# Kernel tuning notes

Measured on AMD Instinct MI355X. Metric: run time of the kernel, lower is better.

Reference implementation:

```python
import jax, jax.numpy as jnp
import numpy as np

N, E, DIN, DL, DOUT, G, K = 50000, 800000, 32, 128, 10, 256, 3


def setup_inputs() -> dict:
    key = jax.random.key(0)
    ks = jax.random.split(key, 24)
    rn = lambda k, s: jax.random.normal(k, s, jnp.float32) * 0.05
    inp = {}
    inp["x"] = jax.random.normal(ks[0], (N, DIN), jnp.float32)
    inp["edge_index"] = jax.random.randint(ks[1], (2, E), 0, N, jnp.int32)
    inp["batch_ids"] = jnp.sort(jax.random.randint(ks[2], (N,), 0, G, jnp.int32))
    inp["y"] = jax.random.uniform(ks[3], (G, DOUT), dtype=jnp.float32)
    inp["eps"] = jax.random.uniform(ks[4], (K, N, DL), dtype=jnp.float32)  # torch.rand_like -> uniform
    inp["W_in"] = rn(ks[5], (DIN, DL)); inp["b_in"] = jnp.zeros((DL,), jnp.float32)
    inp["W_gcn"] = rn(ks[6], (DL, DL)); inp["b_gcn"] = jnp.zeros((DL,), jnp.float32)
    inp["W_enc"] = rn(ks[7], (5, DL, DL)); inp["b_enc"] = jnp.zeros((5, DL), jnp.float32)
    inp["W_mu"] = rn(ks[8], (DL, DL)); inp["b_mu"] = jnp.zeros((DL,), jnp.float32)
    inp["W_std"] = rn(ks[9], (DL, DL)); inp["b_std"] = jnp.zeros((DL,), jnp.float32)
    dims = [DL, 256, 128, 64, 32, 16]
    for i in range(5):
        inp[f"Wd{i}"] = rn(ks[10 + i], (dims[i], dims[i + 1]))
        inp[f"bd{i}"] = jnp.zeros((dims[i + 1],), jnp.float32)
    inp["Wo"] = rn(ks[15], (16, DOUT)); inp["bo"] = jnp.zeros((DOUT,), jnp.float32)
    inp["k"] = K
    return inp


def reference(x, edge_index, batch_ids, y, eps, W_in, b_in, W_gcn, b_gcn,
              W_enc, b_enc, W_mu, b_mu, W_std, b_std,
              Wd0, bd0, Wd1, bd1, Wd2, bd2, Wd3, bd3, Wd4, bd4, Wo, bo, k):
    n = x.shape[0]
    src, dst = edge_index[0], edge_index[1]
    # GCN symmetric normalization with self-loops (PyG gcn_norm, edge_weight=1)
    deg = jnp.zeros((n,), x.dtype).at[dst].add(1.0) + 1.0  # +1 for self-loop
    dinv = jax.lax.rsqrt(deg)
    enorm = (dinv[src] * dinv[dst])[:, None]  # [E,1]
    snorm = (dinv * dinv)[:, None]            # [N,1] self-loop norm

    h = jax.nn.sigmoid(x @ W_in + b_in)  # input layer
    mu = h; std = h
    for i in range(k):  # k hops of MPEncoder (shared weights)
        g = h @ W_gcn  # [N,DL]
        g = jax.ops.segment_sum(g[src] * enorm, dst, num_segments=n) + g * snorm + b_gcn
        for j in range(5):
            g = jax.nn.sigmoid(g @ W_enc[j] + b_enc[j])
        mu = g @ W_mu + b_mu
        std = jax.nn.softplus(g @ W_std + b_std - 5.0)
        h = mu + std * eps[i]  # reparametrization with uniform noise

    # Decoder MLP per node, sigmoid output
    d = h
    for Wd, bd in ((Wd0, bd0), (Wd1, bd1), (Wd2, bd2), (Wd3, bd3), (Wd4, bd4)):
        d = jax.nn.relu(d @ Wd + bd)
    yp = jax.nn.sigmoid(d @ Wo + bo)  # [N,DOUT]

    # global_mean_pool over graphs
    g_count = y.shape[0]
    sums = jax.ops.segment_sum(yp, batch_ids, num_segments=g_count)
    cnt = jax.ops.segment_sum(jnp.ones((n,), yp.dtype), batch_ids, num_segments=g_count)
    y_pred = sums / jnp.maximum(cnt, 1.0)[:, None]
    return (y_pred, mu, std, y)
```

## Files before the change

### kernel.cpp

```cpp
#include <hip/hip_runtime.h>
#include <math.h>

#define DIN 32
#define DL 128
#define DOUT 10

typedef _Float16 f16x8 __attribute__((ext_vector_type(8)));
typedef float f32x4 __attribute__((ext_vector_type(4)));

__device__ __forceinline__ float sigm(float x){ return 1.0f/(1.0f+expf(-x)); }
__device__ __forceinline__ float softplus_(float x){ return fmaxf(x,0.0f) + log1pf(expf(-fabsf(x))); }

__global__ void count_edges_k(const int* __restrict__ ei, int* __restrict__ cnt, int E){
    int e = blockIdx.x*256 + threadIdx.x;
    if (e < E) atomicAdd(&cnt[ei[E + e]], 1);
}

__global__ void dinv_k(const int* __restrict__ cnt, float* __restrict__ dinv, int N){
    int i = blockIdx.x*256 + threadIdx.x;
    if (i < N) dinv[i] = rsqrtf((float)cnt[i] + 1.0f);
}

__global__ void block_sum_k(const int* __restrict__ cnt, int* __restrict__ bsum, int n){
    __shared__ int ws_[4];
    int tid = threadIdx.x;
    int i = blockIdx.x*256 + tid;
    int v = (i < n) ? cnt[i] : 0;
    #pragma unroll
    for (int off = 32; off > 0; off >>= 1) v += __shfl_xor(v, off);
    if ((tid & 63) == 0) ws_[tid >> 6] = v;
    __syncthreads();
    if (tid == 0) bsum[blockIdx.x] = ws_[0] + ws_[1] + ws_[2] + ws_[3];
}

__global__ void scan_bsum_k(int* __restrict__ bsum, int nb){
    __shared__ int tmp[1024];
    int tid = threadIdx.x;
    int v = (tid < nb) ? bsum[tid] : 0;
    tmp[tid] = v; __syncthreads();
    for (int off = 1; off < 1024; off <<= 1){
        int t = (tid >= off) ? tmp[tid-off] : 0;
        __syncthreads();
        tmp[tid] += t;
        __syncthreads();
    }
    if (tid < nb) bsum[tid] = tmp[tid] - v;
}

__global__ void block_scan_k(const int* __restrict__ cnt, const int* __restrict__ bexcl,
                             int* __restrict__ cursor, int* __restrict__ rowptr, int n){
    __shared__ int tmp[256];
    int tid = threadIdx.x;
    int i = blockIdx.x*256 + tid;
    int v = (i < n) ? cnt[i] : 0;
    tmp[tid] = v; __syncthreads();
    for (int off = 1; off < 256; off <<= 1){
        int t = (tid >= off) ? tmp[tid-off] : 0;
        __syncthreads();
        tmp[tid] += t;
        __syncthreads();
    }
    int excl = bexcl[blockIdx.x] + tmp[tid] - v;
    if (i < n){ cursor[i] = excl; rowptr[i+1] = excl + v; }
    if (i == 0) rowptr[0] = 0;
}

__global__ void place_edges_k(const int* __restrict__ ei, int* __restrict__ cursor,
                              int* __restrict__ csr_src, int E){
    int e = blockIdx.x*256 + threadIdx.x;
    if (e < E){
        int s = ei[e], d = ei[E + e];
        csr_src[atomicAdd(&cursor[d], 1)] = s;
    }
}

struct WPA { const float* s; _Float16* d; int K; int C; };
struct WPA14 { WPA a[14]; };
__global__ void wprep_all_k(WPA14 args){
    WPA w = args.a[blockIdx.y];
    int idx = blockIdx.x*256 + threadIdx.x;
    if (idx < w.K*w.C){ int k = idx / w.C, c = idx % w.C; w.d[(size_t)c*w.K + k] = (_Float16)w.s[idx]; }
}

template<int K, int NC16, bool ZERO>
__device__ __forceinline__ void mfma_ldsmm(const _Float16* As, int lda,
        const _Float16* Ws, int ldw, f32x4 (&acc)[2][8], int ln, int q, int wid){
    if (ZERO){
        #pragma unroll
        for (int r = 0; r < 2; ++r)
            #pragma unroll
            for (int c = 0; c < 8; ++c) acc[r][c] = (f32x4){0.f,0.f,0.f,0.f};
    }
    #pragma unroll
    for (int kk = 0; kk < K/32; ++kk){
        int ko = kk*32 + q*8;
        f16x8 a0 = *(const f16x8*)&As[(size_t)(wid*32 + ln)*lda + ko];
        f16x8 a1 = *(const f16x8*)&As[(size_t)(wid*32 + 16 + ln)*lda + ko];
        #pragma unroll
        for (int c = 0; c < NC16; ++c){
            f16x8 b = *(const f16x8*)&Ws[(size_t)(c*16 + ln)*ldw + ko];
            acc[0][c] = __builtin_amdgcn_mfma_f32_16x16x32_f16(a0, b, acc[0][c], 0, 0, 0);
            acc[1][c] = __builtin_amdgcn_mfma_f32_16x16x32_f16(a1, b, acc[1][c], 0, 0, 0);
        }
    }
}

template<int NC16, int ACT>
__device__ __forceinline__ void act_store_lds(_Float16* D, int ldd, f32x4 (&acc)[2][8],
        const float* bias, int ln, int q, int wid){
    #pragma unroll
    for (int r = 0; r < 2; ++r){
        int rowb = wid*32 + r*16 + q*4;
        #pragma unroll
        for (int c = 0; c < NC16; ++c){
            int col = c*16 + ln;
            float bv = bias ? bias[col] : 0.0f;
            #pragma unroll
            for (int i2 = 0; i2 < 4; ++i2){
                float v = acc[r][c][i2] + bv;
                if (ACT == 1) v = sigm(v);
                else if (ACT == 2) v = fmaxf(v, 0.0f);
                D[(size_t)(rowb + i2)*ldd + col] = (_Float16)v;
            }
        }
    }
}

__device__ __forceinline__ void stage_w(const _Float16* Wg, _Float16* Wl, int ldw,
                                        int C, int K, int tid){
    int kq = K/8, tot = C*kq;
    for (int i = tid; i < tot; i += 256){
        int r = i/kq, s = i%kq;
        *(f16x8*)&Wl[(size_t)r*ldw + s*8] = *(const f16x8*)&Wg[(size_t)r*K + s*8];
    }
}

__device__ __forceinline__ void pf_load_w(const _Float16* Wg, f16x8 (&pf)[8], int tid){
    #pragma unroll
    for (int i = 0; i < 8; ++i) pf[i] = *(const f16x8*)&Wg[(size_t)(tid + i*256)*8];
}
__device__ __forceinline__ void pf_store_w(_Float16* Wl, f16x8 (&pf)[8], int tid){
    #pragma unroll
    for (int i = 0; i < 8; ++i){
        int g = tid + i*256; int r = g >> 4, s = g & 15;
        *(f16x8*)&Wl[(size_t)r*136 + s*8] = pf[i];
    }
}

__global__ __launch_bounds__(256,1) void fused_input_k(const float* __restrict__ x,
        const _Float16* __restrict__ WtIN, const float* __restrict__ b_in,
        const _Float16* __restrict__ WtGCN, _Float16* __restrict__ gOut, int nrows){
    __shared__ __align__(16) _Float16 Ax[128*40];
    __shared__ __align__(16) _Float16 Hl[128*136];
    __shared__ __align__(16) _Float16 Wi[128*40];
    __shared__ __align__(16) _Float16 Wg[128*136];
    int tid = threadIdx.x, lane = tid & 63, wid = tid >> 6;
    int ln = lane & 15, q = lane >> 4;
    int row0 = blockIdx.x * 128;
    for (int i = tid; i < 512; i += 256){
        int r = i >> 2, s = i & 3;
        f16x8 v = {};
        if (row0 + r < nrows){
            const float* xs = &x[(size_t)(row0+r)*DIN + s*8];
            float4 u0 = *(const float4*)xs, u1 = *(const float4*)(xs+4);
            v[0]=(_Float16)u0.x; v[1]=(_Float16)u0.y; v[2]=(_Float16)u0.z; v[3]=(_Float16)u0.w;
            v[4]=(_Float16)u1.x; v[5]=(_Float16)u1.y; v[6]=(_Float16)u1.z; v[7]=(_Float16)u1.w;
        }
        *(f16x8*)&Ax[r*40 + s*8] = v;
        *(f16x8*)&Wi[r*40 + s*8] = *(const f16x8*)&WtIN[(size_t)r*32 + s*8];
    }
    for (int i = tid; i < 2048; i += 256){
        int r = i >> 4, s = i & 15;
        *(f16x8*)&Wg[r*136 + s*8] = *(const f16x8*)&WtGCN[(size_t)r*128 + s*8];
    }
    __syncthreads();
    f32x4 acc[2][8];
    mfma_ldsmm<32,8,true>(Ax, 40, Wi, 40, acc, ln, q, wid);
    act_store_lds<8,1>(Hl, 136, acc, b_in, ln, q, wid);
    __syncthreads();
    mfma_ldsmm<128,8,true>(Hl, 136, Wg, 136, acc, ln, q, wid);
    #pragma unroll
    for (int r = 0; r < 2; ++r){
        int rowb = row0 + wid*32 + r*16 + q*4;
        #pragma unroll
        for (int c = 0; c < 8; ++c){
            int col = c*16 + ln;
            #pragma unroll
            for (int i2 = 0; i2 < 4; ++i2){
                int row = rowb + i2;
                if (row < nrows) gOut[(size_t)row*DL + col] = (_Float16)acc[r][c][i2];
            }
        }
    }
}

__global__ __launch_bounds__(256) void gcn_agg_h(const _Float16* __restrict__ g,
        _Float16* __restrict__ out, const int* __restrict__ rowptr,
        const int* __restrict__ csr_src, const float* __restrict__ dinv,
        const float* __restrict__ bgcn, int N){
    int t = threadIdx.x;
    int node = blockIdx.x*16 + (t >> 4);
    int f = (t & 15)*8;
    if (node >= N) return;
    float dv = dinv[node];
    float sn = dv*dv;
    f16x8 sv = *(const f16x8*)&g[(size_t)node*DL + f];
    float acc[8];
    #pragma unroll
    for (int j = 0; j < 8; ++j) acc[j] = (float)sv[j]*sn + bgcn[f+j];
    int e0 = rowptr[node], e1 = rowptr[node+1];
    for (int e = e0; e < e1; ++e){
        int s = csr_src[e];
        float w = dinv[s]*dv;
        f16x8 nv = *(const f16x8*)&g[(size_t)s*DL + f];
        #pragma unroll
        for (int j = 0; j < 8; ++j) acc[j] += (float)nv[j]*w;
    }
    f16x8 o;
    #pragma unroll
    for (int j = 0; j < 8; ++j) o[j] = (_Float16)acc[j];
    *(f16x8*)&out[(size_t)node*DL + f] = o;
}

template<int LAST>
__global__ __launch_bounds__(256,1) void fused_hop_k(const _Float16* __restrict__ g2,
        const _Float16* __restrict__ Wt8, const float* __restrict__ b_enc,
        const float* __restrict__ b_mu, const float* __restrict__ b_std,
        const float* __restrict__ eps_i, _Float16* __restrict__ gOut,
        float* __restrict__ muOut, float* __restrict__ stdOut,
        _Float16* __restrict__ hOut, int nrows){
    __shared__ __align__(16) _Float16 actA[128*136];
    __shared__ __align__(16) _Float16 actB[128*136];
    __shared__ __align__(16) _Float16 wb[2][128*136];
    int tid = threadIdx.x, lane = tid & 63, wid = tid >> 6;
    int ln = lane & 15, q = lane >> 4;
    int row0 = blockIdx.x * 128;
    for (int i = tid; i < 2048; i += 256){
        int r = i >> 4, s = i & 15;
        f16x8 v = {};
        if (row0 + r < nrows) v = *(const f16x8*)&g2[(size_t)(row0+r)*DL + s*8];
        *(f16x8*)&actA[r*136 + s*8] = v;
        *(f16x8*)&wb[0][r*136 + s*8] = *(const f16x8*)&Wt8[(size_t)1*16384 + (size_t)r*128 + s*8];
    }
    __syncthreads();
    _Float16* src = actA; _Float16* dst = actB;
    int cur = 0;
    f32x4 acc[2][8], accS[2][8];
    f16x8 pf[8];
    #pragma unroll 1
    for (int j = 0; j < 5; ++j){
        const _Float16* nxtW = Wt8 + (size_t)((j < 4) ? (2+j) : 6)*16384;
        pf_load_w(nxtW, pf, tid);
        mfma_ldsmm<128,8,true>(src, 136, wb[cur], 136, acc, ln, q, wid);
        pf_store_w(wb[cur^1], pf, tid);
        act_store_lds<8,1>(dst, 136, acc, b_enc + j*DL, ln, q, wid);
        cur ^= 1;
        { _Float16* t = src; src = dst; dst = t; }
        __syncthreads();
    }
    pf_load_w(Wt8 + (size_t)7*16384, pf, tid);
    mfma_ldsmm<128,8,true>(src, 136, wb[cur], 136, acc, ln, q, wid);
    pf_store_w(wb[cur^1], pf, tid);
    cur ^= 1;
    __syncthreads();
    if (!LAST) pf_load_w(Wt8, pf, tid);
    mfma_ldsmm<128,8,true>(src, 136, wb[cur], 136, accS, ln, q, wid);
    if (!LAST) pf_store_w(wb[cur^1], pf, tid);
    cur ^= 1;
    #pragma unroll
    for (int r = 0; r < 2; ++r){
        int rowb = wid*32 + r*16 + q*4;
        #pragma unroll
        for (int c = 0; c < 8; ++c){
            int col = c*16 + ln;
            float bm = b_mu[col], bs = b_std[col];
            #pragma unroll
            for (int i2 = 0; i2 < 4; ++i2){
                int row = rowb + i2;
                int grow = row0 + row;
                float mv = acc[r][c][i2] + bm;
                float sv = softplus_(accS[r][c][i2] + bs - 5.0f);
                float ev = (grow < nrows) ? eps_i[(size_t)grow*DL + col] : 0.0f;
                float hv = mv + sv*ev;
                if (LAST){
                    if (grow < nrows){
                        muOut[(size_t)grow*DL + col] = mv;
                        stdOut[(size_t)grow*DL + col] = sv;
                        hOut[(size_t)grow*DL + col] = (_Float16)hv;
                    }
                } else {
                    dst[(size_t)row*136 + col] = (_Float16)hv;
                }
            }
        }
    }
    if (!LAST){
        __syncthreads();
        mfma_ldsmm<128,8,true>(dst, 136, wb[cur], 136, acc, ln, q, wid);
        #pragma unroll
        for (int r = 0; r < 2; ++r){
            int rowb = row0 + wid*32 + r*16 + q*4;
            #pragma unroll
            for (int c = 0; c < 8; ++c){
                int col = c*16 + ln;
                #pragma unroll
                for (int i2 = 0; i2 < 4; ++i2){
                    int row = rowb + i2;
                    if (row < nrows) gOut[(size_t)row*DL + col] = (_Float16)acc[r][c][i2];
                }
            }
        }
    }
}

__global__ __launch_bounds__(256,1) void decoder_k(const _Float16* __restrict__ h,
        const _Float16* __restrict__ WtD0, const _Float16* __restrict__ WtD1,
        const _Float16* __restrict__ WtD2, const _Float16* __restrict__ WtD3,
        const _Float16* __restrict__ WtD4,
        const float* __restrict__ bd0, const float* __restrict__ bd1,
        const float* __restrict__ bd2, const float* __restrict__ bd3,
        const float* __restrict__ bd4, const float* __restrict__ Wo,
        const float* __restrict__ bo, const int* __restrict__ batch,
        float* __restrict__ sums, float* __restrict__ gcnt, int nrows){
    __shared__ __align__(16) _Float16 A[128*136];
    __shared__ __align__(16) _Float16 B[128*264];
    __shared__ __align__(16) _Float16 W[128*136];
    __shared__ float WoL[16*DOUT];
    __shared__ float boL[DOUT];
    int tid = threadIdx.x, lane = tid & 63, wid = tid >> 6;
    int ln = lane & 15, q = lane >> 4;
    int row0 = blockIdx.x * 128;
    for (int i = tid; i < 2048; i += 256){
        int r = i >> 4, s = i & 15;
        f16x8 v = {};
        if (row0 + r < nrows) v = *(const f16x8*)&h[(size_t)(row0+r)*DL + s*8];
        *(f16x8*)&A[r*136 + s*8] = v;
    }
    if (tid < 16*DOUT) WoL[tid] = Wo[tid];
    if (tid < DOUT) boL[tid] = bo[tid];
    f32x4 acc[2][8];
    for (int ch = 0; ch < 2; ++ch){
        stage_w(WtD0 + (size_t)ch*128*128, W, 136, 128, 128, tid);
        __syncthreads();
        mfma_ldsmm<128,8,true>(A, 136, W, 136, acc, ln, q, wid);
        act_store_lds<8,2>(B + ch*128, 264, acc, bd0 + ch*128, ln, q, wid);
        __syncthreads();
    }
    for (int kh = 0; kh < 2; ++kh){
        for (int i = tid; i < 2048; i += 256){
            int r = i >> 4, s = i & 15;
            *(f16x8*)&W[r*136 + s*8] = *(const f16x8*)&WtD1[(size_t)r*256 + kh*128 + s*8];
        }
        __syncthreads();
        if (kh == 0) mfma_ldsmm<128,8,true >(B,       264, W, 136, acc, ln, q, wid);
        else         mfma_ldsmm<128,8,false>(B + 128, 264, W, 136, acc, ln, q, wid);
        __syncthreads();
    }
    act_store_lds<8,2>(A, 136, acc, bd1, ln, q, wid);
    __syncthreads();
    stage_w(WtD2, W, 136, 64, 128, tid);
    __syncthreads();
    mfma_ldsmm<128,4,true>(A, 136, W, 136, acc, ln, q, wid);
    act_store_lds<4,2>(B, 264, acc, bd2, ln, q, wid);
    __syncthreads();
    stage_w(WtD3, W, 136, 32, 64, tid);
    __syncthreads();
    mfma_ldsmm<64,2,true>(B, 264, W, 136, acc, ln, q, wid);
    act_store_lds<2,2>(A, 136, acc, bd3, ln, q, wid);
    __syncthreads();
    stage_w(WtD4, W, 136, 16, 32, tid);
    __syncthreads();
    mfma_ldsmm<32,1,true>(A, 136, W, 136, acc, ln, q, wid);
    act_store_lds<1,2>(B, 264, acc, bd4, ln, q, wid);
    __syncthreads();
    int node = row0 + tid;
    bool valid = (tid < 128) && (node < nrows);
    float yp[DOUT];
    int b = -1;
    if (valid){
        float dd[16];
        #pragma unroll
        for (int k = 0; k < 16; ++k) dd[k] = (float)B[(size_t)tid*264 + k];
        #pragma unroll
        for (int o = 0; o < DOUT; ++o){
            float a2 = boL[o];
            #pragma unroll
            for (int k = 0; k < 16; ++k) a2 += dd[k]*WoL[k*DOUT + o];
            yp[o] = sigm(a2);
        }
        b = batch[node];
    }
    int b0 = __builtin_amdgcn_readfirstlane(b);
    unsigned long long m = __ballot(b == b0);
    if (m == ~0ull && b0 >= 0){
        #pragma unroll
        for (int o = 0; o < DOUT; ++o){
            float v = yp[o];
            for (int off = 32; off > 0; off >>= 1) v += __shfl_xor(v, off);
            if ((tid & 63) == 0) atomicAdd(&sums[b0*DOUT + o], v);
        }
        if ((tid & 63) == 0) atomicAdd(&gcnt[b0], 64.0f);
    } else if (valid){
        #pragma unroll
        for (int o = 0; o < DOUT; ++o) atomicAdd(&sums[b*DOUT + o], yp[o]);
        atomicAdd(&gcnt[b], 1.0f);
    }
}

__global__ void divide_k(float* __restrict__ out, const float* __restrict__ gcnt, int n){
    int i = blockIdx.x*256 + threadIdx.x;
    if (i < n) out[i] = out[i] / fmaxf(gcnt[i/DOUT], 1.0f);
}

__global__ void copy_k(const float* __restrict__ src, float* __restrict__ dst, int n){
    int i = blockIdx.x*256 + threadIdx.x;
    if (i < n) dst[i] = src[i];
}

extern "C" void kernel_launch(void* const* d_in, const int* in_sizes, int n_in,
                              void* d_out, int out_size, void* d_ws, size_t ws_size,
                              hipStream_t stream) {
    const float* x     = (const float*)d_in[0];
    const int*   ei    = (const int*)d_in[1];
    const int*   batch = (const int*)d_in[2];
    const float* y     = (const float*)d_in[3];
    const float* eps   = (const float*)d_in[4];
    const float* W_in  = (const float*)d_in[5];
    const float* b_in  = (const float*)d_in[6];
    const float* W_gcn = (const float*)d_in[7];
    const float* b_gcn = (const float*)d_in[8];
    const float* W_enc = (const float*)d_in[9];
    const float* b_enc = (const float*)d_in[10];
    const float* W_mu  = (const float*)d_in[11];
    const float* b_mu  = (const float*)d_in[12];
    const float* W_std = (const float*)d_in[13];
    const float* b_std = (const float*)d_in[14];
    const float* Wd0 = (const float*)d_in[15]; const float* bd0 = (const float*)d_in[16];
    const float* Wd1 = (const float*)d_in[17]; const float* bd1 = (const float*)d_in[18];
    const float* Wd2 = (const float*)d_in[19]; const float* bd2 = (const float*)d_in[20];
    const float* Wd3 = (const float*)d_in[21]; const float* bd3 = (const float*)d_in[22];
    const float* Wd4 = (const float*)d_in[23]; const float* bd4 = (const float*)d_in[24];
    const float* Wo  = (const float*)d_in[25]; const float* bo  = (const float*)d_in[26];

    const int N = in_sizes[2];
    const int E = in_sizes[1]/2;
    const int G = in_sizes[3]/DOUT;
    const int KHOP = in_sizes[4] / (N*DL);
    const size_t NN = (size_t)N*DL;

    char* p = (char*)d_ws;
    auto take = [&p](size_t bytes) -> char* {
        char* r = p; p += (bytes + 255) & ~(size_t)255; return r;
    };
    _Float16* hG  = (_Float16*)take(NN*2);
    _Float16* hG2 = (_Float16*)take(NN*2);
    _Float16* hH  = (_Float16*)take(NN*2);
    float* dinv  = (float*)take((size_t)N*4);
    float* gcnt  = (float*)take((size_t)G*4);
    int* cnt     = (int*)take((size_t)N*4);
    int* rowptr  = (int*)take((size_t)(N+1)*4);
    int* cursor  = (int*)take((size_t)N*4);
    int* csr_src = (int*)take((size_t)E*4);
    int* bsum    = (int*)take(1024*4);
    _Float16* Wt8  = (_Float16*)take((size_t)8*DL*DL*2);
    _Float16* WtIN = (_Float16*)take((size_t)DL*DIN*2);
    _Float16* WtD0 = (_Float16*)take((size_t)256*128*2);
    _Float16* WtD1 = (_Float16*)take((size_t)128*256*2);
    _Float16* WtD2 = (_Float16*)take((size_t)64*128*2);
    _Float16* WtD3 = (_Float16*)take((size_t)32*64*2);
    _Float16* WtD4 = (_Float16*)take((size_t)16*32*2);

    float* out_ypred = (float*)d_out;
    float* out_mu    = out_ypred + (size_t)G*DOUT;
    float* out_std   = out_mu + NN;
    float* out_y     = out_std + NN;

    hipMemsetAsync(cnt, 0, sizeof(int)*N, stream);
    hipMemsetAsync(out_ypred, 0, sizeof(float)*G*DOUT, stream);
    hipMemsetAsync(gcnt, 0, sizeof(float)*G, stream);

    int gE = (E + 255)/256, gN = (N + 255)/256;
    int nb = gN;

    count_edges_k<<<gE, 256, 0, stream>>>(ei, cnt, E);
    dinv_k<<<gN, 256, 0, stream>>>(cnt, dinv, N);
    block_sum_k<<<nb, 256, 0, stream>>>(cnt, bsum, N);
    scan_bsum_k<<<1, 1024, 0, stream>>>(bsum, nb);
    block_scan_k<<<nb, 256, 0, stream>>>(cnt, bsum, cursor, rowptr, N);
    place_edges_k<<<gE, 256, 0, stream>>>(ei, cursor, csr_src, E);

    WPA14 wa;
    wa.a[0]  = { W_in,  WtIN, DIN, DL };
    wa.a[1]  = { W_gcn, Wt8,  DL, DL };
    for (int j = 0; j < 5; ++j) wa.a[2+j] = { W_enc + (size_t)j*DL*DL, Wt8 + (size_t)(1+j)*DL*DL, DL, DL };
    wa.a[7]  = { W_mu,  Wt8 + (size_t)6*DL*DL, DL, DL };
    wa.a[8]  = { W_std, Wt8 + (size_t)7*DL*DL, DL, DL };
    wa.a[9]  = { Wd0, WtD0, 128, 256 };
    wa.a[10] = { Wd1, WtD1, 256, 128 };
    wa.a[11] = { Wd2, WtD2, 128, 64 };
    wa.a[12] = { Wd3, WtD3, 64, 32 };
    wa.a[13] = { Wd4, WtD4, 32, 16 };
    wprep_all_k<<<dim3(128, 14), 256, 0, stream>>>(wa);

    int ntile = (N + 127)/128;
    fused_input_k<<<ntile, 256, 0, stream>>>(x, WtIN, b_in, Wt8, hG, N);

    for (int i = 0; i < KHOP; ++i){
        gcn_agg_h<<<(N+15)/16, 256, 0, stream>>>(hG, hG2, rowptr, csr_src, dinv, b_gcn, N);
        const float* eps_i = eps + (size_t)i*NN;
        if (i == KHOP-1)
            fused_hop_k<1><<<ntile, 256, 0, stream>>>(hG2, Wt8, b_enc, b_mu, b_std, eps_i,
                                                      nullptr, out_mu, out_std, hH, N);
        else
            fused_hop_k<0><<<ntile, 256, 0, stream>>>(hG2, Wt8, b_enc, b_mu, b_std, eps_i,
                                                      hG, nullptr, nullptr, nullptr, N);
    }

    decoder_k<<<ntile, 256, 0, stream>>>(hH, WtD0, WtD1, WtD2, WtD3, WtD4,
                                         bd0, bd1, bd2, bd3, bd4, Wo, bo,
                                         batch, out_ypred, gcnt, N);
    divide_k<<<(G*DOUT+255)/256, 256, 0, stream>>>(out_ypred, gcnt, G*DOUT);
    copy_k<<<(G*DOUT+255)/256, 256, 0, stream>>>(y, out_y, G*DOUT);
}
```

Before: 969.8 us.

## Read weights from global memory in MFMA GEMMs and shrink LDS for higher occupancy

The MFMA matmul helper now streams weight fragments straight from global memory (L2-cached) instead of staging them in LDS. This removes the weight LDS buffers and lets the fused input and hop kernels use 512 threads with 4 blocks per CU, each wave computing a 64x32 output tile. The decoder is retiled to 64-row blocks with smaller LDS footprints, and the GCN aggregation unrolls neighbour gathers by four to expose more memory-level parallelism. The cost is repeated global or L2 traffic for weights on every block, and outputs are now staged through LDS before a coalesced copy-out.

```diff
diff --git a/kernel.cpp b/kernel.cpp
--- a/kernel.cpp
+++ b/kernel.cpp
@@ -82,83 +82,91 @@
     if (idx < w.K*w.C){ int k = idx / w.C, c = idx % w.C; w.d[(size_t)c*w.K + k] = (_Float16)w.s[idx]; }
 }
 
-template<int K, int NC16, bool ZERO>
-__device__ __forceinline__ void mfma_ldsmm(const _Float16* As, int lda,
-        const _Float16* Ws, int ldw, f32x4 (&acc)[2][8], int ln, int q, int wid){
+template<int KCH, bool ZERO>
+__device__ __forceinline__ void mm_gw(const _Float16* As, const _Float16* __restrict__ Wt,
+        int ldw, int koff, f32x4 (&acc)[4][2], int ln, int q, int rg, int cg, int ncols){
     if (ZERO){
         #pragma unroll
-        for (int r = 0; r < 2; ++r)
+        for (int mf = 0; mf < 4; ++mf)
             #pragma unroll
-            for (int c = 0; c < 8; ++c) acc[r][c] = (f32x4){0.f,0.f,0.f,0.f};
-    }
-    #pragma unroll
-    for (int kk = 0; kk < K/32; ++kk){
-        int ko = kk*32 + q*8;
-        f16x8 a0 = *(const f16x8*)&As[(size_t)(wid*32 + ln)*lda + ko];
-        f16x8 a1 = *(const f16x8*)&As[(size_t)(wid*32 + 16 + ln)*lda + ko];
-        #pragma unroll
-        for (int c = 0; c < NC16; ++c){
-            f16x8 b = *(const f16x8*)&Ws[(size_t)(c*16 + ln)*ldw + ko];
-            acc[0][c] = __builtin_amdgcn_mfma_f32_16x16x32_f16(a0, b, acc[0][c], 0, 0, 0);
-            acc[1][c] = __builtin_amdgcn_mfma_f32_16x16x32_f16(a1, b, acc[1][c], 0, 0, 0);
-        }
-    }
-}
-
-template<int NC16, int ACT>
-__device__ __forceinline__ void act_store_lds(_Float16* D, int ldd, f32x4 (&acc)[2][8],
-        const float* bias, int ln, int q, int wid){
-    #pragma unroll
-    for (int r = 0; r < 2; ++r){
-        int rowb = wid*32 + r*16 + q*4;
-        #pragma unroll
-        for (int c = 0; c < NC16; ++c){
-            int col = c*16 + ln;
-            float bv = bias ? bias[col] : 0.0f;
+            for (int cf = 0; cf < 2; ++cf) acc[mf][cf] = (f32x4){0.f,0.f,0.f,0.f};
+    }
+    #pragma unroll
+    for (int kk = 0; kk < KCH; ++kk){
+        f16x8 a[4], b[2];
+        #pragma unroll
+        for (int mf = 0; mf < 4; ++mf)
+            a[mf] = *(const f16x8*)&As[(rg*64 + mf*16 + ln)*136 + kk*32 + q*8];
+        #pragma unroll
+        for (int cf = 0; cf < 2; ++cf){
+            int col = cg*32 + cf*16 + ln;
+            if (cg*32 + cf*16 < ncols)
+                b[cf] = *(const f16x8*)&Wt[(size_t)col*ldw + koff + kk*32 + q*8];
+        }
+        #pragma unroll
+        for (int mf = 0; mf < 4; ++mf)
             #pragma unroll
-            for (int i2 = 0; i2 < 4; ++i2){
-                float v = acc[r][c][i2] + bv;
-                if (ACT == 1) v = sigm(v);
-                else if (ACT == 2) v = fmaxf(v, 0.0f);
-                D[(size_t)(rowb + i2)*ldd + col] = (_Float16)v;
+            for (int cf = 0; cf < 2; ++cf)
+                if (cg*32 + cf*16 < ncols)
+                    acc[mf][cf] = __builtin_amdgcn_mfma_f32_16x16x32_f16(a[mf], b[cf], acc[mf][cf], 0, 0, 0);
+    }
+}
+
+template<int ACT>
+__device__ __forceinline__ void act_st(_Float16* D, f32x4 (&acc)[4][2], const float* bias,
+        int ln, int q, int rg, int cg, int ncols){
+    #pragma unroll
+    for (int mf = 0; mf < 4; ++mf){
+        int rowb = rg*64 + mf*16 + q*4;
+        #pragma unroll
+        for (int cf = 0; cf < 2; ++cf){
+            int col = cg*32 + cf*16 + ln;
+            if (cg*32 + cf*16 < ncols){
+                float bv = bias ? bias[col] : 0.0f;
+                #pragma unroll
+                for (int i2 = 0; i2 < 4; ++i2){
+                    float v = acc[mf][cf][i2] + bv;
+                    if (ACT == 1) v = sigm(v);
+                    else if (ACT == 2) v = fmaxf(v, 0.0f);
+                    D[(rowb + i2)*136 + col] = (_Float16)v;
+                }
             }
         }
     }
 }
 
-__device__ __forceinline__ void stage_w(const _Float16* Wg, _Float16* Wl, int ldw,
-                                        int C, int K, int tid){
-    int kq = K/8, tot = C*kq;
-    for (int i = tid; i < tot; i += 256){
-        int r = i/kq, s = i%kq;
-        *(f16x8*)&Wl[(size_t)r*ldw + s*8] = *(const f16x8*)&Wg[(size_t)r*K + s*8];
-    }
-}
-
-__device__ __forceinline__ void pf_load_w(const _Float16* Wg, f16x8 (&pf)[8], int tid){
-    #pragma unroll
-    for (int i = 0; i < 8; ++i) pf[i] = *(const f16x8*)&Wg[(size_t)(tid + i*256)*8];
-}
-__device__ __forceinline__ void pf_store_w(_Float16* Wl, f16x8 (&pf)[8], int tid){
-    #pragma unroll
-    for (int i = 0; i < 8; ++i){
-        int g = tid + i*256; int r = g >> 4, s = g & 15;
-        *(f16x8*)&Wl[(size_t)r*136 + s*8] = pf[i];
-    }
-}
-
-__global__ __launch_bounds__(256,1) void fused_input_k(const float* __restrict__ x,
+template<int NROWT, int NTHR>
+__device__ __forceinline__ void stage_in(const _Float16* __restrict__ Gp, _Float16* S,
+        int row0, int nrows, int tid){
+    for (int i = tid; i < NROWT*16; i += NTHR){
+        int r = i >> 4, s = i & 15;
+        f16x8 v = {};
+        if (row0 + r < nrows) v = *(const f16x8*)&Gp[(size_t)(row0+r)*DL + s*8];
+        *(f16x8*)&S[r*136 + s*8] = v;
+    }
+}
+
+template<int NROWT, int NTHR>
+__device__ __forceinline__ void copy_out(const _Float16* S, _Float16* __restrict__ Gp,
+        int row0, int nrows, int tid){
+    for (int i = tid; i < NROWT*16; i += NTHR){
+        int r = i >> 4, s = i & 15;
+        if (row0 + r < nrows)
+            *(f16x8*)&Gp[(size_t)(row0+r)*DL + s*8] = *(const f16x8*)&S[r*136 + s*8];
+    }
+}
+
+__global__ __launch_bounds__(512,4) void fused_input_k(const float* __restrict__ x,
         const _Float16* __restrict__ WtIN, const float* __restrict__ b_in,
         const _Float16* __restrict__ WtGCN, _Float16* __restrict__ gOut, int nrows){
-    __shared__ __align__(16) _Float16 Ax[128*40];
-    __shared__ __align__(16) _Float16 Hl[128*136];
-    __shared__ __align__(16) _Float16 Wi[128*40];
-    __shared__ __align__(16) _Float16 Wg[128*136];
+    __shared__ __align__(16) _Float16 bufA[128*136];
+    __shared__ __align__(16) _Float16 bufB[128*136];
     int tid = threadIdx.x, lane = tid & 63, wid = tid >> 6;
     int ln = lane & 15, q = lane >> 4;
+    int cg = wid & 3, rg = wid >> 2;
     int row0 = blockIdx.x * 128;
-    for (int i = tid; i < 512; i += 256){
-        int r = i >> 2, s = i & 3;
+    {
+        int r = tid >> 2, s = tid & 3;
         f16x8 v = {};
         if (row0 + r < nrows){
             const float* xs = &x[(size_t)(row0+r)*DIN + s*8];
@@ -166,32 +174,17 @@
             v[0]=(_Float16)u0.x; v[1]=(_Float16)u0.y; v[2]=(_Float16)u0.z; v[3]=(_Float16)u0.w;
             v[4]=(_Float16)u1.x; v[5]=(_Float16)u1.y; v[6]=(_Float16)u1.z; v[7]=(_Float16)u1.w;
         }
-        *(f16x8*)&Ax[r*40 + s*8] = v;
-        *(f16x8*)&Wi[r*40 + s*8] = *(const f16x8*)&WtIN[(size_t)r*32 + s*8];
-    }
-    for (int i = tid; i < 2048; i += 256){
-        int r = i >> 4, s = i & 15;
-        *(f16x8*)&Wg[r*136 + s*8] = *(const f16x8*)&WtGCN[(size_t)r*128 + s*8];
-    }
-    __syncthreads();
-    f32x4 acc[2][8];
-    mfma_ldsmm<32,8,true>(Ax, 40, Wi, 40, acc, ln, q, wid);
-    act_store_lds<8,1>(Hl, 136, acc, b_in, ln, q, wid);
-    __syncthreads();
-    mfma_ldsmm<128,8,true>(Hl, 136, Wg, 136, acc, ln, q, wid);
-    #pragma unroll
-    for (int r = 0; r < 2; ++r){
-        int rowb = row0 + wid*32 + r*16 + q*4;
-        #pragma unroll
-        for (int c = 0; c < 8; ++c){
-            int col = c*16 + ln;
-            #pragma unroll
-            for (int i2 = 0; i2 < 4; ++i2){
-                int row = rowb + i2;
-                if (row < nrows) gOut[(size_t)row*DL + col] = (_Float16)acc[r][c][i2];
-            }
-        }
-    }
+        *(f16x8*)&bufA[r*136 + s*8] = v;
+    }
+    __syncthreads();
+    f32x4 acc[4][2];
+    mm_gw<1,true>(bufA, WtIN, DIN, 0, acc, ln, q, rg, cg, 128);
+    act_st<1>(bufB, acc, b_in, ln, q, rg, cg, 128);
+    __syncthreads();
+    mm_gw<4,true>(bufB, WtGCN, DL, 0, acc, ln, q, rg, cg, 128);
+    act_st<0>(bufA, acc, nullptr, ln, q, rg, cg, 128);
+    __syncthreads();
+    copy_out<128,512>(bufA, gOut, row0, nrows, tid);
 }
 
 __global__ __launch_bounds__(256) void gcn_agg_h(const _Float16* __restrict__ g,
@@ -208,8 +201,19 @@
     float acc[8];
     #pragma unroll
     for (int j = 0; j < 8; ++j) acc[j] = (float)sv[j]*sn + bgcn[f+j];
-    int e0 = rowptr[node], e1 = rowptr[node+1];
-    for (int e = e0; e < e1; ++e){
+    int e = rowptr[node], e1 = rowptr[node+1];
+    for (; e + 4 <= e1; e += 4){
+        int s0 = csr_src[e], s1 = csr_src[e+1], s2 = csr_src[e+2], s3 = csr_src[e+3];
+        float w0 = dinv[s0]*dv, w1 = dinv[s1]*dv, w2 = dinv[s2]*dv, w3 = dinv[s3]*dv;
+        f16x8 n0 = *(const f16x8*)&g[(size_t)s0*DL + f];
+        f16x8 n1 = *(const f16x8*)&g[(size_t)s1*DL + f];
+        f16x8 n2 = *(const f16x8*)&g[(size_t)s2*DL + f];
+        f16x8 n3 = *(const f16x8*)&g[(size_t)s3*DL + f];
+        #pragma unroll
+        for (int j = 0; j < 8; ++j)
+            acc[j] += (float)n0[j]*w0 + (float)n1[j]*w1 + (float)n2[j]*w2 + (float)n3[j]*w3;
+    }
+    for (; e < e1; ++e){
         int s = csr_src[e];
         float w = dinv[s]*dv;
         f16x8 nv = *(const f16x8*)&g[(size_t)s*DL + f];
@@ -223,97 +227,82 @@
 }
 
 template<int LAST>
-__global__ __launch_bounds__(256,1) void fused_hop_k(const _Float16* __restrict__ g2,
+__global__ __launch_bounds__(512,4) void fused_hop_k(const _Float16* __restrict__ g2,
         const _Float16* __restrict__ Wt8, const float* __restrict__ b_enc,
         const float* __restrict__ b_mu, const float* __restrict__ b_std,
         const float* __restrict__ eps_i, _Float16* __restrict__ gOut,
         float* __restrict__ muOut, float* __restrict__ stdOut,
         _Float16* __restrict__ hOut, int nrows){
-    __shared__ __align__(16) _Float16 actA[128*136];
-    __shared__ __align__(16) _Float16 actB[128*136];
-    __shared__ __align__(16) _Float16 wb[2][128*136];
+    __shared__ __align__(16) _Float16 bufA[128*136];
+    __shared__ __align__(16) _Float16 bufB[128*136];
     int tid = threadIdx.x, lane = tid & 63, wid = tid >> 6;
     int ln = lane & 15, q = lane >> 4;
+    int cg = wid & 3, rg = wid >> 2;
     int row0 = blockIdx.x * 128;
-    for (int i = tid; i < 2048; i += 256){
-        int r = i >> 4, s = i & 15;
-        f16x8 v = {};
-        if (row0 + r < nrows) v = *(const f16x8*)&g2[(size_t)(row0+r)*DL + s*8];
-        *(f16x8*)&actA[r*136 + s*8] = v;
-        *(f16x8*)&wb[0][r*136 + s*8] = *(const f16x8*)&Wt8[(size_t)1*16384 + (size_t)r*128 + s*8];
-    }
-    __syncthreads();
-    _Float16* src = actA; _Float16* dst = actB;
-    int cur = 0;
-    f32x4 acc[2][8], accS[2][8];
-    f16x8 pf[8];
+    stage_in<128,512>(g2, bufA, row0, nrows, tid);
+    __syncthreads();
+    _Float16* src = bufA; _Float16* dst = bufB;
+    f32x4 acc[4][2];
     #pragma unroll 1
     for (int j = 0; j < 5; ++j){
-        const _Float16* nxtW = Wt8 + (size_t)((j < 4) ? (2+j) : 6)*16384;
-        pf_load_w(nxtW, pf, tid);
-        mfma_ldsmm<128,8,true>(src, 136, wb[cur], 136, acc, ln, q, wid);
-        pf_store_w(wb[cur^1], pf, tid);
-        act_store_lds<8,1>(dst, 136, acc, b_enc + j*DL, ln, q, wid);
-        cur ^= 1;
-        { _Float16* t = src; src = dst; dst = t; }
-        __syncthreads();
-    }
-    pf_load_w(Wt8 + (size_t)7*16384, pf, tid);
-    mfma_ldsmm<128,8,true>(src, 136, wb[cur], 136, acc, ln, q, wid);
-    pf_store_w(wb[cur^1], pf, tid);
-    cur ^= 1;
-    __syncthreads();
-    if (!LAST) pf_load_w(Wt8, pf, tid);
-    mfma_ldsmm<128,8,true>(src, 136, wb[cur], 136, accS, ln, q, wid);
-    if (!LAST) pf_store_w(wb[cur^1], pf, tid);
-    cur ^= 1;
-    #pragma unroll
-    for (int r = 0; r < 2; ++r){
-        int rowb = wid*32 + r*16 + q*4;
-        #pragma unroll
-        for (int c = 0; c < 8; ++c){
-            int col = c*16 + ln;
-            float bm = b_mu[col], bs = b_std[col];
+        mm_gw<4,true>(src, Wt8 + (size_t)(1+j)*16384, DL, 0, acc, ln, q, rg, cg, 128);
+        act_st<1>(dst, acc, b_enc + j*DL, ln, q, rg, cg, 128);
+        __syncthreads();
+        { _Float16* tt = src; src = dst; dst = tt; }
+    }
+    _Float16 svr[4][2][4];
+    mm_gw<4,true>(src, Wt8 + (size_t)7*16384, DL, 0, acc, ln, q, rg, cg, 128);
+    #pragma unroll
+    for (int mf = 0; mf < 4; ++mf){
+        int rowb = rg*64 + mf*16 + q*4;
+        #pragma unroll
+        for (int cf = 0; cf < 2; ++cf){
+            int col = cg*32 + cf*16 + ln;
+            float bs = b_std[col];
+            #pragma unroll
+            for (int i2 = 0; i2 < 4; ++i2){
+                float s = softplus_(acc[mf][cf][i2] + bs - 5.0f);
+                svr[mf][cf][i2] = (_Float16)s;
+                if (LAST){
+                    int grow = row0 + rowb + i2;
+                    if (grow < nrows) stdOut[(size_t)grow*DL + col] = s;
+                }
+            }
+        }
+    }
+    mm_gw<4,true>(src, Wt8 + (size_t)6*16384, DL, 0, acc, ln, q, rg, cg, 128);
+    __syncthreads();
+    #pragma unroll
+    for (int mf = 0; mf < 4; ++mf){
+        int rowb = rg*64 + mf*16 + q*4;
+        #pragma unroll
+        for (int cf = 0; cf < 2; ++cf){
+            int col = cg*32 + cf*16 + ln;
+            float bm = b_mu[col];
             #pragma unroll
             for (int i2 = 0; i2 < 4; ++i2){
                 int row = rowb + i2;
                 int grow = row0 + row;
-                float mv = acc[r][c][i2] + bm;
-                float sv = softplus_(accS[r][c][i2] + bs - 5.0f);
+                float mv = acc[mf][cf][i2] + bm;
                 float ev = (grow < nrows) ? eps_i[(size_t)grow*DL + col] : 0.0f;
-                float hv = mv + sv*ev;
-                if (LAST){
-                    if (grow < nrows){
-                        muOut[(size_t)grow*DL + col] = mv;
-                        stdOut[(size_t)grow*DL + col] = sv;
-                        hOut[(size_t)grow*DL + col] = (_Float16)hv;
-                    }
-                } else {
-                    dst[(size_t)row*136 + col] = (_Float16)hv;
-                }
+                float hv = mv + (float)svr[mf][cf][i2]*ev;
+                dst[row*136 + col] = (_Float16)hv;
+                if (LAST && grow < nrows) muOut[(size_t)grow*DL + col] = mv;
             }
         }
     }
-    if (!LAST){
-        __syncthreads();
-        mfma_ldsmm<128,8,true>(dst, 136, wb[cur], 136, acc, ln, q, wid);
-        #pragma unroll
-        for (int r = 0; r < 2; ++r){
-            int rowb = row0 + wid*32 + r*16 + q*4;
-            #pragma unroll
-            for (int c = 0; c < 8; ++c){
-                int col = c*16 + ln;
-                #pragma unroll
-                for (int i2 = 0; i2 < 4; ++i2){
-                    int row = rowb + i2;
-                    if (row < nrows) gOut[(size_t)row*DL + col] = (_Float16)acc[r][c][i2];
-                }
-            }
-        }
-    }
-}
-
-__global__ __launch_bounds__(256,1) void decoder_k(const _Float16* __restrict__ h,
+    __syncthreads();
+    if (LAST){
+        copy_out<128,512>(dst, hOut, row0, nrows, tid);
+    } else {
+        mm_gw<4,true>(dst, Wt8, DL, 0, acc, ln, q, rg, cg, 128);
+        act_st<0>(src, acc, nullptr, ln, q, rg, cg, 128);
+        __syncthreads();
+        copy_out<128,512>(src, gOut, row0, nrows, tid);
+    }
+}
+
+__global__ __launch_bounds__(256,3) void decoder_k(const _Float16* __restrict__ h,
         const _Float16* __restrict__ WtD0, const _Float16* __restrict__ WtD1,
         const _Float16* __restrict__ WtD2, const _Float16* __restrict__ WtD3,
         const _Float16* __restrict__ WtD4,
@@ -322,65 +311,47 @@
         const float* __restrict__ bd4, const float* __restrict__ Wo,
         const float* __restrict__ bo, const int* __restrict__ batch,
         float* __restrict__ sums, float* __restrict__ gcnt, int nrows){
-    __shared__ __align__(16) _Float16 A[128*136];
-    __shared__ __align__(16) _Float16 B[128*264];
-    __shared__ __align__(16) _Float16 W[128*136];
+    __shared__ __align__(16) _Float16 A[64*136];
+    __shared__ __align__(16) _Float16 B0[64*136];
+    __shared__ __align__(16) _Float16 B1[64*136];
     __shared__ float WoL[16*DOUT];
     __shared__ float boL[DOUT];
     int tid = threadIdx.x, lane = tid & 63, wid = tid >> 6;
     int ln = lane & 15, q = lane >> 4;
-    int row0 = blockIdx.x * 128;
-    for (int i = tid; i < 2048; i += 256){
-        int r = i >> 4, s = i & 15;
-        f16x8 v = {};
-        if (row0 + r < nrows) v = *(const f16x8*)&h[(size_t)(row0+r)*DL + s*8];
-        *(f16x8*)&A[r*136 + s*8] = v;
-    }
+    int cg = wid, rg = 0;
+    int row0 = blockIdx.x * 64;
+    stage_in<64,256>(h, A, row0, nrows, tid);
     if (tid < 16*DOUT) WoL[tid] = Wo[tid];
     if (tid < DOUT) boL[tid] = bo[tid];
-    f32x4 acc[2][8];
-    for (int ch = 0; ch < 2; ++ch){
-        stage_w(WtD0 + (size_t)ch*128*128, W, 136, 128, 128, tid);
-        __syncthreads();
-        mfma_ldsmm<128,8,true>(A, 136, W, 136, acc, ln, q, wid);
-        act_store_lds<8,2>(B + ch*128, 264, acc, bd0 + ch*128, ln, q, wid);
-        __syncthreads();
-    }
-    for (int kh = 0; kh < 2; ++kh){
-        for (int i = tid; i < 2048; i += 256){
-            int r = i >> 4, s = i & 15;
-            *(f16x8*)&W[r*136 + s*8] = *(const f16x8*)&WtD1[(size_t)r*256 + kh*128 + s*8];
-        }
-        __syncthreads();
-        if (kh == 0) mfma_ldsmm<128,8,true >(B,       264, W, 136, acc, ln, q, wid);
-        else         mfma_ldsmm<128,8,false>(B + 128, 264, W, 136, acc, ln, q, wid);
-        __syncthreads();
-    }
-    act_store_lds<8,2>(A, 136, acc, bd1, ln, q, wid);
-    __syncthreads();
-    stage_w(WtD2, W, 136, 64, 128, tid);
-    __syncthreads();
-    mfma_ldsmm<128,4,true>(A, 136, W, 136, acc, ln, q, wid);
-    act_store_lds<4,2>(B, 264, acc, bd2, ln, q, wid);
-    __syncthreads();
-    stage_w(WtD3, W, 136, 32, 64, tid);
-    __syncthreads();
-    mfma_ldsmm<64,2,true>(B, 264, W, 136, acc, ln, q, wid);
-    act_store_lds<2,2>(A, 136, acc, bd3, ln, q, wid);
-    __syncthreads();
-    stage_w(WtD4, W, 136, 16, 32, tid);
-    __syncthreads();
-    mfma_ldsmm<32,1,true>(A, 136, W, 136, acc, ln, q, wid);
-    act_store_lds<1,2>(B, 264, acc, bd4, ln, q, wid);
+    __syncthreads();
+    f32x4 acc[4][2];
+    mm_gw<4,true>(A, WtD0, 128, 0, acc, ln, q, rg, cg, 128);
+    act_st<2>(B0, acc, bd0, ln, q, rg, cg, 128);
+    __syncthreads();
+    mm_gw<4,true>(A, WtD0 + (size_t)128*128, 128, 0, acc, ln, q, rg, cg, 128);
+    act_st<2>(B1, acc, bd0 + 128, ln, q, rg, cg, 128);
+    __syncthreads();
+    mm_gw<4,true >(B0, WtD1, 256, 0,   acc, ln, q, rg, cg, 128);
+    mm_gw<4,false>(B1, WtD1, 256, 128, acc, ln, q, rg, cg, 128);
+    act_st<2>(A, acc, bd1, ln, q, rg, cg, 128);
+    __syncthreads();
+    mm_gw<4,true>(A, WtD2, 128, 0, acc, ln, q, rg, cg, 64);
+    act_st<2>(B0, acc, bd2, ln, q, rg, cg, 64);
+    __syncthreads();
+    mm_gw<2,true>(B0, WtD3, 64, 0, acc, ln, q, rg, cg, 32);
+    act_st<2>(A, acc, bd3, ln, q, rg, cg, 32);
+    __syncthreads();
+    mm_gw<1,true>(A, WtD4, 32, 0, acc, ln, q, rg, cg, 16);
+    act_st<2>(B0, acc, bd4, ln, q, rg, cg, 16);
     __syncthreads();
     int node = row0 + tid;
-    bool valid = (tid < 128) && (node < nrows);
+    bool valid = (tid < 64) && (node < nrows);
     float yp[DOUT];
     int b = -1;
     if (valid){
         float dd[16];
         #pragma unroll
-        for (int k = 0; k < 16; ++k) dd[k] = (float)B[(size_t)tid*264 + k];
+        for (int k = 0; k < 16; ++k) dd[k] = (float)B0[tid*136 + k];
         #pragma unroll
         for (int o = 0; o < DOUT; ++o){
             float a2 = boL[o];
@@ -503,22 +474,22 @@
     wprep_all_k<<<dim3(128, 14), 256, 0, stream>>>(wa);
 
     int ntile = (N + 127)/128;
-    fused_input_k<<<ntile, 256, 0, stream>>>(x, WtIN, b_in, Wt8, hG, N);
+    fused_input_k<<<ntile, 512, 0, stream>>>(x, WtIN, b_in, Wt8, hG, N);
 
     for (int i = 0; i < KHOP; ++i){
         gcn_agg_h<<<(N+15)/16, 256, 0, stream>>>(hG, hG2, rowptr, csr_src, dinv, b_gcn, N);
         const float* eps_i = eps + (size_t)i*NN;
         if (i == KHOP-1)
-            fused_hop_k<1><<<ntile, 256, 0, stream>>>(hG2, Wt8, b_enc, b_mu, b_std, eps_i,
+            fused_hop_k<1><<<ntile, 512, 0, stream>>>(hG2, Wt8, b_enc, b_mu, b_std, eps_i,
                                                       nullptr, out_mu, out_std, hH, N);
         else
-            fused_hop_k<0><<<ntile, 256, 0, stream>>>(hG2, Wt8, b_enc, b_mu, b_std, eps_i,
+            fused_hop_k<0><<<ntile, 512, 0, stream>>>(hG2, Wt8, b_enc, b_mu, b_std, eps_i,
                                                       hG, nullptr, nullptr, nullptr, N);
     }
 
-    decoder_k<<<ntile, 256, 0, stream>>>(hH, WtD0, WtD1, WtD2, WtD3, WtD4,
-                                         bd0, bd1, bd2, bd3, bd4, Wo, bo,
-                                         batch, out_ypred, gcnt, N);
+    decoder_k<<<(N+63)/64, 256, 0, stream>>>(hH, WtD0, WtD1, WtD2, WtD3, WtD4,
+                                             bd0, bd1, bd2, bd3, bd4, Wo, bo,
+                                             batch, out_ypred, gcnt, N);
     divide_k<<<(G*DOUT+255)/256, 256, 0, stream>>>(out_ypred, gcnt, G*DOUT);
     copy_k<<<(G*DOUT+255)/256, 256, 0, stream>>>(y, out_y, G*DOUT);
 }
```

After: 1.412 ms. 45.6% more time.

## Restructure hop MLP kernel to per-wave row tiles with higher occupancy

Applied to the files above, without the earlier changes.

Replaces the 256-thread fused hop kernel, which used double-buffered weights and two full activation tiles, with a 512-thread kernel. Each of the 8 waves owns 16 rows in a private LDS scratch, and all waves share a single weight buffer staged with syncthreads. The smaller LDS footprint and launch bounds of 512 with 4 blocks per CU are meant to raise occupancy. The trade is losing the weight prefetch overlap and adding barriers before and after each weight stage. The GCN aggregation loop is also unrolled by four edges to put more gathers in flight.

```diff
diff --git a/kernel.cpp b/kernel.cpp
--- a/kernel.cpp
+++ b/kernel.cpp
@@ -132,18 +132,6 @@
     for (int i = tid; i < tot; i += 256){
         int r = i/kq, s = i%kq;
         *(f16x8*)&Wl[(size_t)r*ldw + s*8] = *(const f16x8*)&Wg[(size_t)r*K + s*8];
-    }
-}
-
-__device__ __forceinline__ void pf_load_w(const _Float16* Wg, f16x8 (&pf)[8], int tid){
-    #pragma unroll
-    for (int i = 0; i < 8; ++i) pf[i] = *(const f16x8*)&Wg[(size_t)(tid + i*256)*8];
-}
-__device__ __forceinline__ void pf_store_w(_Float16* Wl, f16x8 (&pf)[8], int tid){
-    #pragma unroll
-    for (int i = 0; i < 8; ++i){
-        int g = tid + i*256; int r = g >> 4, s = g & 15;
-        *(f16x8*)&Wl[(size_t)r*136 + s*8] = pf[i];
     }
 }
 
@@ -208,8 +196,19 @@
     float acc[8];
     #pragma unroll
     for (int j = 0; j < 8; ++j) acc[j] = (float)sv[j]*sn + bgcn[f+j];
-    int e0 = rowptr[node], e1 = rowptr[node+1];
-    for (int e = e0; e < e1; ++e){
+    int e = rowptr[node], e1 = rowptr[node+1];
+    for (; e + 4 <= e1; e += 4){
+        int s0 = csr_src[e], s1 = csr_src[e+1], s2 = csr_src[e+2], s3 = csr_src[e+3];
+        float w0 = dinv[s0]*dv, w1 = dinv[s1]*dv, w2 = dinv[s2]*dv, w3 = dinv[s3]*dv;
+        f16x8 n0 = *(const f16x8*)&g[(size_t)s0*DL + f];
+        f16x8 n1 = *(const f16x8*)&g[(size_t)s1*DL + f];
+        f16x8 n2 = *(const f16x8*)&g[(size_t)s2*DL + f];
+        f16x8 n3 = *(const f16x8*)&g[(size_t)s3*DL + f];
+        #pragma unroll
+        for (int j = 0; j < 8; ++j)
+            acc[j] += (float)n0[j]*w0 + (float)n1[j]*w1 + (float)n2[j]*w2 + (float)n3[j]*w3;
+    }
+    for (; e < e1; ++e){
         int s = csr_src[e];
         float w = dinv[s]*dv;
         f16x8 nv = *(const f16x8*)&g[(size_t)s*DL + f];
@@ -223,92 +222,126 @@
 }
 
 template<int LAST>
-__global__ __launch_bounds__(256,1) void fused_hop_k(const _Float16* __restrict__ g2,
+__global__ __launch_bounds__(512,4) void hop_reg_k(const _Float16* __restrict__ g2,
         const _Float16* __restrict__ Wt8, const float* __restrict__ b_enc,
         const float* __restrict__ b_mu, const float* __restrict__ b_std,
         const float* __restrict__ eps_i, _Float16* __restrict__ gOut,
         float* __restrict__ muOut, float* __restrict__ stdOut,
         _Float16* __restrict__ hOut, int nrows){
-    __shared__ __align__(16) _Float16 actA[128*136];
-    __shared__ __align__(16) _Float16 actB[128*136];
-    __shared__ __align__(16) _Float16 wb[2][128*136];
+    __shared__ __align__(16) _Float16 Wb[128*136];
+    __shared__ __align__(16) _Float16 Sc[8*16*136];
     int tid = threadIdx.x, lane = tid & 63, wid = tid >> 6;
     int ln = lane & 15, q = lane >> 4;
-    int row0 = blockIdx.x * 128;
-    for (int i = tid; i < 2048; i += 256){
-        int r = i >> 4, s = i & 15;
+    int row0 = blockIdx.x*128;
+    _Float16* mySc = Sc + wid*16*136;
+    int wrow0 = row0 + wid*16;
+
+    #pragma unroll
+    for (int i = 0; i < 4; ++i){
+        int gg = lane + i*64;
+        int r = gg >> 4, s = gg & 15;
         f16x8 v = {};
-        if (row0 + r < nrows) v = *(const f16x8*)&g2[(size_t)(row0+r)*DL + s*8];
-        *(f16x8*)&actA[r*136 + s*8] = v;
-        *(f16x8*)&wb[0][r*136 + s*8] = *(const f16x8*)&Wt8[(size_t)1*16384 + (size_t)r*128 + s*8];
-    }
-    __syncthreads();
-    _Float16* src = actA; _Float16* dst = actB;
-    int cur = 0;
-    f32x4 acc[2][8], accS[2][8];
-    f16x8 pf[8];
+        if (wrow0 + r < nrows) v = *(const f16x8*)&g2[(size_t)(wrow0+r)*DL + s*8];
+        *(f16x8*)&mySc[r*136 + s*8] = v;
+    }
+
+    f32x4 acc[8];
+    _Float16 svr[8][4];
+
+    auto stageW = [&](int m){
+        __syncthreads();
+        const _Float16* Wg = Wt8 + (size_t)m*16384;
+        #pragma unroll
+        for (int i = 0; i < 4; ++i){
+            int gg = tid + i*512;
+            int r = gg >> 4, s = gg & 15;
+            *(f16x8*)&Wb[r*136 + s*8] = *(const f16x8*)&Wg[(size_t)r*128 + s*8];
+        }
+        __syncthreads();
+    };
+    auto gemm = [&](){
+        #pragma unroll
+        for (int c = 0; c < 8; ++c) acc[c] = (f32x4){0.f,0.f,0.f,0.f};
+        #pragma unroll
+        for (int kk = 0; kk < 4; ++kk){
+            f16x8 a = *(const f16x8*)&mySc[ln*136 + kk*32 + q*8];
+            #pragma unroll
+            for (int c = 0; c < 8; ++c){
+                f16x8 b = *(const f16x8*)&Wb[(c*16 + ln)*136 + kk*32 + q*8];
+                acc[c] = __builtin_amdgcn_mfma_f32_16x16x32_f16(a, b, acc[c], 0, 0, 0);
+            }
+        }
+    };
+
     #pragma unroll 1
     for (int j = 0; j < 5; ++j){
-        const _Float16* nxtW = Wt8 + (size_t)((j < 4) ? (2+j) : 6)*16384;
-        pf_load_w(nxtW, pf, tid);
-        mfma_ldsmm<128,8,true>(src, 136, wb[cur], 136, acc, ln, q, wid);
-        pf_store_w(wb[cur^1], pf, tid);
-        act_store_lds<8,1>(dst, 136, acc, b_enc + j*DL, ln, q, wid);
-        cur ^= 1;
-        { _Float16* t = src; src = dst; dst = t; }
-        __syncthreads();
-    }
-    pf_load_w(Wt8 + (size_t)7*16384, pf, tid);
-    mfma_ldsmm<128,8,true>(src, 136, wb[cur], 136, acc, ln, q, wid);
-    pf_store_w(wb[cur^1], pf, tid);
-    cur ^= 1;
-    __syncthreads();
-    if (!LAST) pf_load_w(Wt8, pf, tid);
-    mfma_ldsmm<128,8,true>(src, 136, wb[cur], 136, accS, ln, q, wid);
-    if (!LAST) pf_store_w(wb[cur^1], pf, tid);
-    cur ^= 1;
-    #pragma unroll
-    for (int r = 0; r < 2; ++r){
-        int rowb = wid*32 + r*16 + q*4;
+        stageW(1+j);
+        gemm();
         #pragma unroll
         for (int c = 0; c < 8; ++c){
             int col = c*16 + ln;
-            float bm = b_mu[col], bs = b_std[col];
-            #pragma unroll
-            for (int i2 = 0; i2 < 4; ++i2){
-                int row = rowb + i2;
-                int grow = row0 + row;
-                float mv = acc[r][c][i2] + bm;
-                float sv = softplus_(accS[r][c][i2] + bs - 5.0f);
-                float ev = (grow < nrows) ? eps_i[(size_t)grow*DL + col] : 0.0f;
-                float hv = mv + sv*ev;
-                if (LAST){
-                    if (grow < nrows){
-                        muOut[(size_t)grow*DL + col] = mv;
-                        stdOut[(size_t)grow*DL + col] = sv;
-                        hOut[(size_t)grow*DL + col] = (_Float16)hv;
-                    }
-                } else {
-                    dst[(size_t)row*136 + col] = (_Float16)hv;
-                }
+            float bv = b_enc[j*DL + col];
+            #pragma unroll
+            for (int i2 = 0; i2 < 4; ++i2)
+                mySc[(q*4+i2)*136 + col] = (_Float16)sigm(acc[c][i2] + bv);
+        }
+    }
+    stageW(7);
+    gemm();
+    #pragma unroll
+    for (int c = 0; c < 8; ++c){
+        int col = c*16 + ln;
+        float bs = b_std[col];
+        #pragma unroll
+        for (int i2 = 0; i2 < 4; ++i2){
+            float s = softplus_(acc[c][i2] + bs - 5.0f);
+            svr[c][i2] = (_Float16)s;
+            if (LAST){
+                int grow = wrow0 + q*4 + i2;
+                if (grow < nrows) stdOut[(size_t)grow*DL + col] = s;
             }
         }
     }
-    if (!LAST){
-        __syncthreads();
-        mfma_ldsmm<128,8,true>(dst, 136, wb[cur], 136, acc, ln, q, wid);
-        #pragma unroll
-        for (int r = 0; r < 2; ++r){
-            int rowb = row0 + wid*32 + r*16 + q*4;
-            #pragma unroll
-            for (int c = 0; c < 8; ++c){
-                int col = c*16 + ln;
-                #pragma unroll
-                for (int i2 = 0; i2 < 4; ++i2){
-                    int row = rowb + i2;
-                    if (row < nrows) gOut[(size_t)row*DL + col] = (_Float16)acc[r][c][i2];
-                }
-            }
+    stageW(6);
+    gemm();
+    #pragma unroll
+    for (int c = 0; c < 8; ++c){
+        int col = c*16 + ln;
+        float bm = b_mu[col];
+        #pragma unroll
+        for (int i2 = 0; i2 < 4; ++i2){
+            int grow = wrow0 + q*4 + i2;
+            float mv = acc[c][i2] + bm;
+            float ev = (grow < nrows) ? eps_i[(size_t)grow*DL + col] : 0.0f;
+            float hv = mv + (float)svr[c][i2]*ev;
+            mySc[(q*4+i2)*136 + col] = (_Float16)hv;
+            if (LAST && grow < nrows) muOut[(size_t)grow*DL + col] = mv;
+        }
+    }
+    if (LAST){
+        #pragma unroll
+        for (int i = 0; i < 4; ++i){
+            int gg = lane + i*64;
+            int r = gg >> 4, s = gg & 15;
+            if (wrow0 + r < nrows)
+                *(f16x8*)&hOut[(size_t)(wrow0+r)*DL + s*8] = *(const f16x8*)&mySc[r*136 + s*8];
+        }
+    } else {
+        stageW(0);
+        gemm();
+        #pragma unroll
+        for (int c = 0; c < 8; ++c){
+            int col = c*16 + ln;
+            #pragma unroll
+            for (int i2 = 0; i2 < 4; ++i2)
+                mySc[(q*4+i2)*136 + col] = (_Float16)acc[c][i2];
+        }
+        #pragma unroll
+        for (int i = 0; i < 4; ++i){
+            int gg = lane + i*64;
+            int r = gg >> 4, s = gg & 15;
+            if (wrow0 + r < nrows)
+                *(f16x8*)&gOut[(size_t)(wrow0+r)*DL + s*8] = *(const f16x8*)&mySc[r*136 + s*8];
         }
     }
 }
@@ -509,11 +542,11 @@
         gcn_agg_h<<<(N+15)/16, 256, 0, stream>>>(hG, hG2, rowptr, csr_src, dinv, b_gcn, N);
         const float* eps_i = eps + (size_t)i*NN;
         if (i == KHOP-1)
-            fused_hop_k<1><<<ntile, 256, 0, stream>>>(hG2, Wt8, b_enc, b_mu, b_std, eps_i,
-                                                      nullptr, out_mu, out_std, hH, N);
+            hop_reg_k<1><<<ntile, 512, 0, stream>>>(hG2, Wt8, b_enc, b_mu, b_std, eps_i,
+                                                    nullptr, out_mu, out_std, hH, N);
         else
-            fused_hop_k<0><<<ntile, 256, 0, stream>>>(hG2, Wt8, b_enc, b_mu, b_std, eps_i,
-                                                      hG, nullptr, nullptr, nullptr, N);
+            hop_reg_k<0><<<ntile, 512, 0, stream>>>(hG2, Wt8, b_enc, b_mu, b_std, eps_i,
+                                                    hG, nullptr, nullptr, nullptr, N);
     }
 
     decoder_k<<<ntile, 256, 0, stream>>>(hH, WtD0, WtD1, WtD2, WtD3, WtD4,
```

Result: slower. 1.108 ms (+14.2%).
